# Kernel optimization log

Hardware: AMD Instinct MI355X
Metric: run time of the kernel (lower is better)

## Reference

```python
import jax, jax.numpy as jnp
import numpy as np

N_NODES = 100000


def _gcn_norm(src, dst, n_nodes, n_edges):
    # PyG gcn_norm with add_self_loops=False: deg over target (col) index
    ones = jnp.ones((n_edges,), dtype=jnp.float32)
    deg = jax.ops.segment_sum(ones, dst, num_segments=n_nodes)
    dinv = jnp.where(deg > 0, jax.lax.rsqrt(deg), 0.0)
    return dinv[src] * dinv[dst]  # [E]


def _arma_conv(x, src, dst, ew, init_w, root_w, bias, n_nodes):
    # x: [N, Fin]; init_w/root_w: [K, Fin, Fout]; bias: [K, 1, Fout]
    h = jnp.einsum('nf,kfo->kno', x, init_w)          # [K, N, Fout]
    msg = h[:, src, :] * ew[None, :, None]             # [K, E, Fout]
    agg = jax.vmap(lambda m: jax.ops.segment_sum(m, dst, num_segments=n_nodes))(msg)
    out = agg + jnp.einsum('nf,kfo->kno', x, root_w) + bias
    return jax.nn.relu(out).mean(axis=0)               # mean over stacks K


def setup_inputs() -> dict:
    key = jax.random.key(0)
    ks = jax.random.split(key, 8)
    n, e = N_NODES, 3200000
    nfeat, hid, nclass, K = 512, 16, 40, 2
    x = jax.random.normal(ks[0], (n, nfeat), dtype=jnp.float32)
    edge_index = jax.random.randint(ks[1], (2, e), 0, n, dtype=jnp.int32)
    s1 = (1.0 / np.sqrt(nfeat)).astype(np.float32) if isinstance(np.sqrt(nfeat), np.ndarray) else np.float32(1.0 / np.sqrt(nfeat))
    s2 = np.float32(1.0 / np.sqrt(hid))
    iw1 = jax.random.normal(ks[2], (K, nfeat, hid), dtype=jnp.float32) * s1
    rw1 = jax.random.normal(ks[3], (K, nfeat, hid), dtype=jnp.float32) * s1
    b1 = jax.random.normal(ks[4], (K, 1, hid), dtype=jnp.float32) * 0.01
    iw2 = jax.random.normal(ks[5], (K, hid, nclass), dtype=jnp.float32) * s2
    rw2 = jax.random.normal(ks[6], (K, hid, nclass), dtype=jnp.float32) * s2
    b2 = jax.random.normal(ks[7], (K, 1, nclass), dtype=jnp.float32) * 0.01
    return {'x': x, 'edge_index': edge_index, 'iw1': iw1, 'rw1': rw1, 'b1': b1,
            'iw2': iw2, 'rw2': rw2, 'b2': b2}


def reference(x, edge_index, iw1, rw1, b1, iw2, rw2, b2):
    src, dst = edge_index[0], edge_index[1]
    n = N_NODES
    ew = _gcn_norm(src, dst, n, src.shape[0])
    h = _arma_conv(x, src, dst, ew, iw1, rw1, b1, n)   # [N, 16]
    out = _arma_conv(h, src, dst, ew, iw2, rw2, b2, n) # [N, nclass]
    return out
```

## Files before the change

kernel.cpp:

```cpp
#include <hip/hip_runtime.h>


#define TB 256
#define CHA 4096

typedef __attribute__((ext_vector_type(8))) short bf8;
typedef __attribute__((ext_vector_type(4))) float f4;

__device__ inline unsigned short f2bf_rne(float f) {
  unsigned int u = __float_as_uint(f);
  unsigned int r = u + 0x7fffu + ((u >> 16) & 1u);
  return (unsigned short)(r >> 16);
}
__device__ inline float bf2f(unsigned short h) {
  return __uint_as_float(((unsigned int)h) << 16);
}
__device__ inline float bflo(unsigned int u) { return __uint_as_float(u << 16); }
__device__ inline float bfhi(unsigned int u) { return __uint_as_float(u & 0xffff0000u); }
__device__ inline unsigned int bfpack(float lo, float hi) {
  return (unsigned int)f2bf_rne(lo) | ((unsigned int)f2bf_rne(hi) << 16);
}

__global__ __launch_bounds__(TB) void k_countA(const int* __restrict__ dst,
                                               int* __restrict__ ccnt, int E) {
  __shared__ int cnt[256];
  int tid = threadIdx.x;
  cnt[tid] = 0;
  __syncthreads();
  int e0 = blockIdx.x * CHA;
  int e1 = min(e0 + CHA, E);
  for (int e = e0 + tid; e < e1; e += TB) atomicAdd(&cnt[dst[e] >> 9], 1);
  __syncthreads();
  if (cnt[tid] > 0) atomicAdd(&ccnt[tid], cnt[tid]);
}

__global__ __launch_bounds__(256) void k_scanC(const int* __restrict__ ccnt,
                                               int* __restrict__ cbase,
                                               int* __restrict__ ccur) {
  __shared__ int sh[256];
  int tid = threadIdx.x;
  int v = ccnt[tid];
  sh[tid] = v;
  __syncthreads();
  for (int d = 1; d < 256; d <<= 1) {
    int t = (tid >= d) ? sh[tid - d] : 0;
    __syncthreads();
    sh[tid] += t;
    __syncthreads();
  }
  int excl = sh[tid] - v;
  cbase[tid] = excl;
  ccur[tid] = excl;
  if (tid == 255) cbase[256] = sh[255];
}

__global__ __launch_bounds__(TB) void k_binA(const int* __restrict__ src,
                                             const int* __restrict__ dst,
                                             int* __restrict__ ccur,
                                             int2* __restrict__ epairs, int E) {
  __shared__ int cnt[256];
  __shared__ int gb[256];
  int tid = threadIdx.x;
  cnt[tid] = 0;
  __syncthreads();
  int e0 = blockIdx.x * CHA;
  int e1 = min(e0 + CHA, E);
  for (int e = e0 + tid; e < e1; e += TB) atomicAdd(&cnt[dst[e] >> 9], 1);
  __syncthreads();
  int c = cnt[tid];
  if (c > 0) gb[tid] = atomicAdd(&ccur[tid], c);
  __syncthreads();
  cnt[tid] = 0;
  __syncthreads();
  for (int e = e0 + tid; e < e1; e += TB) {
    int dv = dst[e];
    int b = dv >> 9;
    int r = atomicAdd(&cnt[b], 1);
    epairs[gb[b] + r] = make_int2(src[e], dv);
  }
}

__global__ __launch_bounds__(TB) void k_binB(const int2* __restrict__ epairs,
                                             const int* __restrict__ cbase,
                                             int* __restrict__ degi,
                                             int* __restrict__ offsets,
                                             int* __restrict__ srcs, int N) {
  __shared__ int cnt[512];
  __shared__ int pre[512];
  int b = blockIdx.x;
  int n0 = b << 9;
  int tid = threadIdx.x;
  int beg = cbase[b], end = cbase[b + 1];
  int i0 = tid, i1 = tid + 256;
  cnt[i0] = 0; cnt[i1] = 0;
  __syncthreads();
  for (int e = beg + tid; e < end; e += TB) atomicAdd(&cnt[epairs[e].y - n0], 1);
  __syncthreads();
  pre[i0] = cnt[i0]; pre[i1] = cnt[i1];
  __syncthreads();
  for (int d = 1; d < 512; d <<= 1) {
    int t0 = (i0 >= d) ? pre[i0 - d] : 0;
    int t1 = (i1 >= d) ? pre[i1 - d] : 0;
    __syncthreads();
    pre[i0] += t0; pre[i1] += t1;
    __syncthreads();
  }
  int e0 = pre[i0] - cnt[i0];
  int e1x = pre[i1] - cnt[i1];
  if (n0 + i0 < N) { degi[n0 + i0] = cnt[i0]; offsets[n0 + i0] = beg + e0; }
  if (n0 + i1 < N) { degi[n0 + i1] = cnt[i1]; offsets[n0 + i1] = beg + e1x; }
  __syncthreads();
  cnt[i0] = e0; cnt[i1] = e1x;
  __syncthreads();
  for (int e = beg + tid; e < end; e += TB) {
    int2 p = epairs[e];
    int pos = atomicAdd(&cnt[p.y - n0], 1);
    srcs[beg + pos] = p.x;
  }
}

__global__ __launch_bounds__(TB) void k_dinv(const int* __restrict__ degi,
                                             float* __restrict__ dinv, int N) {
  int i = blockIdx.x * TB + threadIdx.x;
  if (i < N) {
    int d = degi[i];
    dinv[i] = d > 0 ? rsqrtf((float)d) : 0.0f;
  }
}

__global__ __launch_bounds__(TB) void k_wsplit(const float* __restrict__ iw1,
                                               const float* __restrict__ rw1,
                                               short* __restrict__ Whi,
                                               short* __restrict__ Wlo) {
  int idx = blockIdx.x * TB + threadIdx.x;
  if (idx >= 32768) return;
  int j = idx & 7;
  int l = (idx >> 3) & 63;
  int t = (idx >> 9) & 3;
  int c = idx >> 11;
  int k = c * 32 + (l >> 4) * 8 + j;
  int n = t * 16 + (l & 15);
  float w;
  if (n < 16)
    w = iw1[k * 16 + n];
  else if (n < 32)
    w = iw1[8192 + k * 16 + (n - 16)];
  else if (n < 48)
    w = rw1[k * 16 + (n - 32)];
  else
    w = rw1[8192 + k * 16 + (n - 48)];
  unsigned short h = f2bf_rne(w);
  float res = w - bf2f(h);
  Whi[idx] = (short)h;
  Wlo[idx] = (short)f2bf_rne(res);
}

__global__ __launch_bounds__(TB) void k_gemm1_mfma(const float* __restrict__ x,
                                                   const short* __restrict__ Whi,
                                                   const short* __restrict__ Wlo,
                                                   const float* __restrict__ dinv,
                                                   unsigned short* __restrict__ Hs,
                                                   float* __restrict__ R, int N) {
  int lane = threadIdx.x & 63;
  int wave = threadIdx.x >> 6;
  int row0 = blockIdx.x * 64 + wave * 16;
  int m = lane & 15, quad = lane >> 4;
  int r = row0 + m;
  bool rv = (r < N);
  const float* xr = x + (size_t)r * 512;

  f4 acc[4];
#pragma unroll
  for (int t = 0; t < 4; t++) acc[t] = (f4){0.f, 0.f, 0.f, 0.f};

  for (int c = 0; c < 16; ++c) {
    float xv[8];
    if (rv) {
      f4 a0 = *(const f4*)(xr + c * 32 + quad * 8);
      f4 a1 = *(const f4*)(xr + c * 32 + quad * 8 + 4);
      xv[0] = a0.x; xv[1] = a0.y; xv[2] = a0.z; xv[3] = a0.w;
      xv[4] = a1.x; xv[5] = a1.y; xv[6] = a1.z; xv[7] = a1.w;
    } else {
#pragma unroll
      for (int j = 0; j < 8; ++j) xv[j] = 0.f;
    }
    bf8 ahi, alo;
#pragma unroll
    for (int j = 0; j < 8; ++j) {
      unsigned short h = f2bf_rne(xv[j]);
      float res = xv[j] - bf2f(h);
      ahi[j] = (short)h;
      alo[j] = (short)f2bf_rne(res);
    }
    const short* wb = Whi + ((size_t)(c * 4) * 64 + lane) * 8;
    const short* wl = Wlo + ((size_t)(c * 4) * 64 + lane) * 8;
#pragma unroll
    for (int t = 0; t < 4; ++t) {
      bf8 bh = *(const bf8*)(wb + t * 512);
      bf8 bl = *(const bf8*)(wl + t * 512);
      acc[t] = __builtin_amdgcn_mfma_f32_16x16x32_bf16(ahi, bh, acc[t], 0, 0, 0);
      acc[t] = __builtin_amdgcn_mfma_f32_16x16x32_bf16(alo, bh, acc[t], 0, 0, 0);
      acc[t] = __builtin_amdgcn_mfma_f32_16x16x32_bf16(ahi, bl, acc[t], 0, 0, 0);
    }
  }
  float dv[4];
#pragma unroll
  for (int g = 0; g < 4; ++g) {
    int ro = row0 + quad * 4 + g;
    dv[g] = (ro < N) ? dinv[ro] : 0.f;
  }
#pragma unroll
  for (int t = 0; t < 4; ++t) {
#pragma unroll
    for (int g = 0; g < 4; ++g) {
      int ro = row0 + quad * 4 + g;
      if (ro < N) {
        if (t < 2)
          Hs[(size_t)ro * 32 + t * 16 + m] = f2bf_rne(acc[t][g] * dv[g]);
        else
          R[(size_t)ro * 32 + (t - 2) * 16 + m] = acc[t][g];
      }
    }
  }
}

__global__ __launch_bounds__(TB) void k_prop1(const int* __restrict__ offsets,
                                              const int* __restrict__ degi,
                                              const int* __restrict__ srcs,
                                              const unsigned short* __restrict__ Hs,
                                              const float* __restrict__ R,
                                              const float* __restrict__ dinv,
                                              const float* __restrict__ b1,
                                              float* __restrict__ h,
                                              unsigned short* __restrict__ hs, int N) {
  int tid = blockIdx.x * TB + threadIdx.x;
  int q = tid & 3;
  int n = tid >> 2;
  if (n >= N) return;
  int beg = offsets[n], cnt = degi[n];
  float a[8];
#pragma unroll
  for (int j = 0; j < 8; j++) a[j] = 0.f;
  for (int i = 0; i < cnt; i++) {
    int s = srcs[beg + i];
    uint4 v = *(const uint4*)(Hs + (size_t)s * 32 + q * 8);
    a[0] += bflo(v.x); a[1] += bfhi(v.x);
    a[2] += bflo(v.y); a[3] += bfhi(v.y);
    a[4] += bflo(v.z); a[5] += bfhi(v.z);
    a[6] += bflo(v.w); a[7] += bfhi(v.w);
  }
  float dvn = dinv[n];
  f4 r0 = *(const f4*)(R + (size_t)n * 32 + q * 8);
  f4 r1 = *(const f4*)(R + (size_t)n * 32 + q * 8 + 4);
  float rr[8] = {r0.x, r0.y, r0.z, r0.w, r1.x, r1.y, r1.z, r1.w};
  float vv[8];
#pragma unroll
  for (int j = 0; j < 8; j++) {
    int f = q * 8 + j;
    vv[j] = fmaxf(a[j] * dvn + rr[j] + b1[(f >> 4) * 16 + (f & 15)], 0.f);
  }
  float pv[8];
#pragma unroll
  for (int j = 0; j < 8; j++) pv[j] = __shfl_xor(vv[j], 2);
  if (q < 2) {
    float hv[8];
#pragma unroll
    for (int j = 0; j < 8; j++) hv[j] = 0.5f * (vv[j] + pv[j]);
    f4 o0 = {hv[0], hv[1], hv[2], hv[3]};
    f4 o1 = {hv[4], hv[5], hv[6], hv[7]};
    *(f4*)(h + (size_t)n * 16 + q * 8) = o0;
    *(f4*)(h + (size_t)n * 16 + q * 8 + 4) = o1;
    uint4 ob;
    ob.x = bfpack(hv[0] * dvn, hv[1] * dvn);
    ob.y = bfpack(hv[2] * dvn, hv[3] * dvn);
    ob.z = bfpack(hv[4] * dvn, hv[5] * dvn);
    ob.w = bfpack(hv[6] * dvn, hv[7] * dvn);
    *(uint4*)(hs + (size_t)n * 16 + q * 8) = ob;
  }
}

__global__ __launch_bounds__(TB) void k_prop2(const int* __restrict__ offsets,
                                              const int* __restrict__ degi,
                                              const int* __restrict__ srcs,
                                              const unsigned short* __restrict__ hs,
                                              const float* __restrict__ dinv,
                                              float* __restrict__ Ah, int N) {
  int tid = blockIdx.x * TB + threadIdx.x;
  int q = tid & 3;
  int n = tid >> 2;
  if (n >= N) return;
  int beg = offsets[n], cnt = degi[n];
  float a[4] = {0.f, 0.f, 0.f, 0.f};
  for (int i = 0; i < cnt; i++) {
    int s = srcs[beg + i];
    uint2 v = *(const uint2*)(hs + (size_t)s * 16 + q * 4);
    a[0] += bflo(v.x); a[1] += bfhi(v.x);
    a[2] += bflo(v.y); a[3] += bfhi(v.y);
  }
  float dvn = dinv[n];
  f4 o = {a[0] * dvn, a[1] * dvn, a[2] * dvn, a[3] * dvn};
  *(f4*)(Ah + (size_t)n * 16 + q * 4) = o;
}

__global__ __launch_bounds__(TB) void k_final(const float* __restrict__ Ah,
                                              const float* __restrict__ h,
                                              const float* __restrict__ iw2,
                                              const float* __restrict__ rw2,
                                              const float* __restrict__ b2,
                                              float* __restrict__ out, int N) {
  __shared__ float w_iw[2 * 16 * 40];
  __shared__ float w_rw[2 * 16 * 40];
  __shared__ float w_b[2 * 40];
  for (int i = threadIdx.x; i < 1280; i += TB) {
    w_iw[i] = iw2[i];
    w_rw[i] = rw2[i];
  }
  for (int i = threadIdx.x; i < 80; i += TB) w_b[i] = b2[i];
  __syncthreads();

  int idx = blockIdx.x * TB + threadIdx.x;
  if (idx >= N * 40) return;
  int n = idx / 40;
  int o = idx - n * 40;
  float a[16], hr[16];
#pragma unroll
  for (int f = 0; f < 16; f++) {
    a[f] = Ah[(size_t)n * 16 + f];
    hr[f] = h[(size_t)n * 16 + f];
  }
  float res = 0.f;
#pragma unroll
  for (int k = 0; k < 2; k++) {
    float s = w_b[k * 40 + o];
#pragma unroll
    for (int f = 0; f < 16; f++) {
      s += a[f] * w_iw[(k * 16 + f) * 40 + o];
      s += hr[f] * w_rw[(k * 16 + f) * 40 + o];
    }
    res += fmaxf(s, 0.f);
  }
  out[idx] = 0.5f * res;
}

extern "C" void kernel_launch(void* const* d_in, const int* in_sizes, int n_in,
                              void* d_out, int out_size, void* d_ws, size_t ws_size,
                              hipStream_t stream) {
  const float* x = (const float*)d_in[0];
  const int* ei = (const int*)d_in[1];
  const float* iw1 = (const float*)d_in[2];
  const float* rw1 = (const float*)d_in[3];
  const float* b1 = (const float*)d_in[4];
  const float* iw2 = (const float*)d_in[5];
  const float* rw2 = (const float*)d_in[6];
  const float* b2 = (const float*)d_in[7];
  float* out = (float*)d_out;

  const int N = in_sizes[0] / 512;
  const int E = in_sizes[1] / 2;
  const int* src = ei;
  const int* dst = ei + E;
  const int NC = (N + 511) >> 9;

  char* base = (char*)d_ws;
  size_t off = 0;
  auto alloc = [&](size_t bytes) -> void* {
    off = (off + 255) & ~(size_t)255;
    void* p = base + off;
    off += bytes;
    return p;
  };
  int* degi = (int*)alloc((size_t)N * 4);
  float* dinv = (float*)alloc((size_t)N * 4);
  int* offsets = (int*)alloc((size_t)N * 4);
  int* ccnt = (int*)alloc(260 * 4);
  int* cbase = (int*)alloc(260 * 4);
  int* ccur = (int*)alloc(260 * 4);
  int2* epairs = (int2*)alloc((size_t)E * 8);
  int* srcs = (int*)alloc((size_t)E * 4);
  unsigned short* Hs = (unsigned short*)alloc((size_t)N * 32 * 2);
  float* hbuf = (float*)alloc((size_t)N * 16 * 4);
  unsigned short* hs = (unsigned short*)alloc((size_t)N * 16 * 2);
  float* Ah = (float*)alloc((size_t)N * 16 * 4);
  short* Whi = (short*)alloc(32768 * 2);
  short* Wlo = (short*)alloc(32768 * 2);
  float* R = (float*)epairs;
  (void)ws_size;

  hipMemsetAsync(ccnt, 0, 260 * 4, stream);

  int NBLK = (E + CHA - 1) / CHA;
  k_countA<<<NBLK, TB, 0, stream>>>(dst, ccnt, E);
  k_scanC<<<1, 256, 0, stream>>>(ccnt, cbase, ccur);
  k_binA<<<NBLK, TB, 0, stream>>>(src, dst, ccur, epairs, E);
  k_binB<<<NC, TB, 0, stream>>>(epairs, cbase, degi, offsets, srcs, N);
  k_dinv<<<(N + TB - 1) / TB, TB, 0, stream>>>(degi, dinv, N);
  k_wsplit<<<128, TB, 0, stream>>>(iw1, rw1, Whi, Wlo);
  k_gemm1_mfma<<<(N + 63) / 64, TB, 0, stream>>>(x, Whi, Wlo, dinv, Hs, R, N);
  k_prop1<<<((size_t)N * 4 + TB - 1) / TB, TB, 0, stream>>>(offsets, degi, srcs, Hs, R,
                                                            dinv, b1, hbuf, hs, N);
  k_prop2<<<((size_t)N * 4 + TB - 1) / TB, TB, 0, stream>>>(offsets, degi, srcs, hs,
                                                            dinv, Ah, N);
  k_final<<<((size_t)N * 40 + TB - 1) / TB, TB, 0, stream>>>(Ah, hbuf, iw2, rw2, b2, out, N);
}
```

Baseline: 604.2 us.

## Pack edge bins to 32-bit, split CSR scatter, stage neighbor lists in LDS

Each binned edge is now stored as one 32-bit word (local destination in the high bits, source in the low bits) instead of an int2, which halves the binning traffic. The per-bucket scatter moves out of the single-block kernel into a separate 2D-grid kernel that uses global per-node atomic cursors. The degree-inverse computation is folded into the histogram kernel, and R gets its own buffer instead of aliasing the edge buffer. The propagation kernels stage each 64-node block's neighbor indices in LDS and unroll the gather by four for more loads in flight. The risks are that edge order within a node becomes nondeterministic, which can change the float summation order, and that the packing assumes node ids fit in 23 bits.

Measured after the change: 606.7 us. About the same (+0.4%).

```diff
diff --git a/kernel.cpp b/kernel.cpp
--- a/kernel.cpp
+++ b/kernel.cpp
@@ -3,6 +3,7 @@
 
 #define TB 256
 #define CHA 4096
+#define SCAP 4096
 
 typedef __attribute__((ext_vector_type(8))) short bf8;
 typedef __attribute__((ext_vector_type(4))) float f4;
@@ -19,6 +20,16 @@
 __device__ inline float bfhi(unsigned int u) { return __uint_as_float(u & 0xffff0000u); }
 __device__ inline unsigned int bfpack(float lo, float hi) {
   return (unsigned int)f2bf_rne(lo) | ((unsigned int)f2bf_rne(hi) << 16);
+}
+__device__ inline void acc8(float* a, uint4 v) {
+  a[0] += bflo(v.x); a[1] += bfhi(v.x);
+  a[2] += bflo(v.y); a[3] += bfhi(v.y);
+  a[4] += bflo(v.z); a[5] += bfhi(v.z);
+  a[6] += bflo(v.w); a[7] += bfhi(v.w);
+}
+__device__ inline void acc4(float* a, uint2 v) {
+  a[0] += bflo(v.x); a[1] += bfhi(v.x);
+  a[2] += bflo(v.y); a[3] += bfhi(v.y);
 }
 
 __global__ __launch_bounds__(TB) void k_countA(const int* __restrict__ dst,
@@ -57,7 +68,7 @@
 __global__ __launch_bounds__(TB) void k_binA(const int* __restrict__ src,
                                              const int* __restrict__ dst,
                                              int* __restrict__ ccur,
-                                             int2* __restrict__ epairs, int E) {
+                                             unsigned int* __restrict__ epack, int E) {
   __shared__ int cnt[256];
   __shared__ int gb[256];
   int tid = threadIdx.x;
@@ -76,15 +87,16 @@
     int dv = dst[e];
     int b = dv >> 9;
     int r = atomicAdd(&cnt[b], 1);
-    epairs[gb[b] + r] = make_int2(src[e], dv);
-  }
-}
-
-__global__ __launch_bounds__(TB) void k_binB(const int2* __restrict__ epairs,
+    epack[gb[b] + r] = ((unsigned int)(dv & 511) << 23) | (unsigned int)src[e];
+  }
+}
+
+__global__ __launch_bounds__(TB) void k_hist(const unsigned int* __restrict__ epack,
                                              const int* __restrict__ cbase,
                                              int* __restrict__ degi,
                                              int* __restrict__ offsets,
-                                             int* __restrict__ srcs, int N) {
+                                             int* __restrict__ cursor,
+                                             float* __restrict__ dinv, int N) {
   __shared__ int cnt[512];
   __shared__ int pre[512];
   int b = blockIdx.x;
@@ -94,7 +106,7 @@
   int i0 = tid, i1 = tid + 256;
   cnt[i0] = 0; cnt[i1] = 0;
   __syncthreads();
-  for (int e = beg + tid; e < end; e += TB) atomicAdd(&cnt[epairs[e].y - n0], 1);
+  for (int e = beg + tid; e < end; e += TB) atomicAdd(&cnt[epack[e] >> 23], 1);
   __syncthreads();
   pre[i0] = cnt[i0]; pre[i1] = cnt[i1];
   __syncthreads();
@@ -107,24 +119,34 @@
   }
   int e0 = pre[i0] - cnt[i0];
   int e1x = pre[i1] - cnt[i1];
-  if (n0 + i0 < N) { degi[n0 + i0] = cnt[i0]; offsets[n0 + i0] = beg + e0; }
-  if (n0 + i1 < N) { degi[n0 + i1] = cnt[i1]; offsets[n0 + i1] = beg + e1x; }
-  __syncthreads();
-  cnt[i0] = e0; cnt[i1] = e1x;
-  __syncthreads();
-  for (int e = beg + tid; e < end; e += TB) {
-    int2 p = epairs[e];
-    int pos = atomicAdd(&cnt[p.y - n0], 1);
-    srcs[beg + pos] = p.x;
-  }
-}
-
-__global__ __launch_bounds__(TB) void k_dinv(const int* __restrict__ degi,
-                                             float* __restrict__ dinv, int N) {
-  int i = blockIdx.x * TB + threadIdx.x;
-  if (i < N) {
-    int d = degi[i];
-    dinv[i] = d > 0 ? rsqrtf((float)d) : 0.0f;
+  if (n0 + i0 < N) {
+    int c = cnt[i0];
+    degi[n0 + i0] = c; offsets[n0 + i0] = beg + e0; cursor[n0 + i0] = beg + e0;
+    dinv[n0 + i0] = c > 0 ? rsqrtf((float)c) : 0.f;
+  }
+  if (n0 + i1 < N) {
+    int c = cnt[i1];
+    degi[n0 + i1] = c; offsets[n0 + i1] = beg + e1x; cursor[n0 + i1] = beg + e1x;
+    dinv[n0 + i1] = c > 0 ? rsqrtf((float)c) : 0.f;
+  }
+}
+
+__global__ __launch_bounds__(TB) void k_scat(const unsigned int* __restrict__ epack,
+                                             const int* __restrict__ cbase,
+                                             int* __restrict__ cursor,
+                                             int* __restrict__ srcs) {
+  int b = blockIdx.x;
+  int beg = cbase[b], end = cbase[b + 1];
+  int len = end - beg;
+  int ny = (int)gridDim.y;
+  int chunk = (len + ny - 1) / ny;
+  int lo = beg + blockIdx.y * chunk;
+  int hi = min(lo + chunk, end);
+  for (int e = lo + (int)threadIdx.x; e < hi; e += TB) {
+    unsigned int v = epack[e];
+    int node = (b << 9) + (int)(v >> 23);
+    int pos = atomicAdd(&cursor[node], 1);
+    srcs[pos] = (int)(v & 0x7FFFFFu);
   }
 }
 
@@ -232,22 +254,53 @@
                                               const float* __restrict__ dinv,
                                               const float* __restrict__ b1,
                                               float* __restrict__ h,
-                                              unsigned short* __restrict__ hs, int N) {
-  int tid = blockIdx.x * TB + threadIdx.x;
+                                              unsigned short* __restrict__ hs,
+                                              int N, int E) {
+  __shared__ int sh[SCAP];
+  int n0 = blockIdx.x * 64;
+  int tid = threadIdx.x;
   int q = tid & 3;
-  int n = tid >> 2;
+  int n = n0 + (tid >> 2);
+  int beg0 = offsets[n0];
+  int end0 = (n0 + 64 < N) ? offsets[n0 + 64] : E;
+  int seg = end0 - beg0;
+  bool lds_ok = (seg <= SCAP);
+  if (lds_ok) {
+    for (int i = tid; i < seg; i += TB) sh[i] = srcs[beg0 + i];
+  }
+  __syncthreads();
   if (n >= N) return;
   int beg = offsets[n], cnt = degi[n];
-  float a[8];
-#pragma unroll
-  for (int j = 0; j < 8; j++) a[j] = 0.f;
-  for (int i = 0; i < cnt; i++) {
-    int s = srcs[beg + i];
-    uint4 v = *(const uint4*)(Hs + (size_t)s * 32 + q * 8);
-    a[0] += bflo(v.x); a[1] += bfhi(v.x);
-    a[2] += bflo(v.y); a[3] += bfhi(v.y);
-    a[4] += bflo(v.z); a[5] += bfhi(v.z);
-    a[6] += bflo(v.w); a[7] += bfhi(v.w);
+  const unsigned short* Hsq = Hs + q * 8;
+  float a[8] = {0.f, 0.f, 0.f, 0.f, 0.f, 0.f, 0.f, 0.f};
+  int i = 0;
+  if (lds_ok) {
+    int ib = beg - beg0;
+    for (; i + 4 <= cnt; i += 4) {
+      int s0 = sh[ib + i], s1 = sh[ib + i + 1], s2 = sh[ib + i + 2], s3 = sh[ib + i + 3];
+      uint4 v0 = *(const uint4*)(Hsq + (size_t)s0 * 32);
+      uint4 v1 = *(const uint4*)(Hsq + (size_t)s1 * 32);
+      uint4 v2 = *(const uint4*)(Hsq + (size_t)s2 * 32);
+      uint4 v3 = *(const uint4*)(Hsq + (size_t)s3 * 32);
+      acc8(a, v0); acc8(a, v1); acc8(a, v2); acc8(a, v3);
+    }
+    for (; i < cnt; i++) {
+      uint4 v = *(const uint4*)(Hsq + (size_t)sh[ib + i] * 32);
+      acc8(a, v);
+    }
+  } else {
+    for (; i + 4 <= cnt; i += 4) {
+      int s0 = srcs[beg + i], s1 = srcs[beg + i + 1], s2 = srcs[beg + i + 2], s3 = srcs[beg + i + 3];
+      uint4 v0 = *(const uint4*)(Hsq + (size_t)s0 * 32);
+      uint4 v1 = *(const uint4*)(Hsq + (size_t)s1 * 32);
+      uint4 v2 = *(const uint4*)(Hsq + (size_t)s2 * 32);
+      uint4 v3 = *(const uint4*)(Hsq + (size_t)s3 * 32);
+      acc8(a, v0); acc8(a, v1); acc8(a, v2); acc8(a, v3);
+    }
+    for (; i < cnt; i++) {
+      uint4 v = *(const uint4*)(Hsq + (size_t)srcs[beg + i] * 32);
+      acc8(a, v);
+    }
   }
   float dvn = dinv[n];
   f4 r0 = *(const f4*)(R + (size_t)n * 32 + q * 8);
@@ -255,10 +308,8 @@
   float rr[8] = {r0.x, r0.y, r0.z, r0.w, r1.x, r1.y, r1.z, r1.w};
   float vv[8];
 #pragma unroll
-  for (int j = 0; j < 8; j++) {
-    int f = q * 8 + j;
-    vv[j] = fmaxf(a[j] * dvn + rr[j] + b1[(f >> 4) * 16 + (f & 15)], 0.f);
-  }
+  for (int j = 0; j < 8; j++)
+    vv[j] = fmaxf(a[j] * dvn + rr[j] + b1[q * 8 + j], 0.f);
   float pv[8];
 #pragma unroll
   for (int j = 0; j < 8; j++) pv[j] = __shfl_xor(vv[j], 2);
@@ -284,18 +335,52 @@
                                               const int* __restrict__ srcs,
                                               const unsigned short* __restrict__ hs,
                                               const float* __restrict__ dinv,
-                                              float* __restrict__ Ah, int N) {
-  int tid = blockIdx.x * TB + threadIdx.x;
+                                              float* __restrict__ Ah, int N, int E) {
+  __shared__ int sh[SCAP];
+  int n0 = blockIdx.x * 64;
+  int tid = threadIdx.x;
   int q = tid & 3;
-  int n = tid >> 2;
+  int n = n0 + (tid >> 2);
+  int beg0 = offsets[n0];
+  int end0 = (n0 + 64 < N) ? offsets[n0 + 64] : E;
+  int seg = end0 - beg0;
+  bool lds_ok = (seg <= SCAP);
+  if (lds_ok) {
+    for (int i = tid; i < seg; i += TB) sh[i] = srcs[beg0 + i];
+  }
+  __syncthreads();
   if (n >= N) return;
   int beg = offsets[n], cnt = degi[n];
+  const unsigned short* hq = hs + q * 4;
   float a[4] = {0.f, 0.f, 0.f, 0.f};
-  for (int i = 0; i < cnt; i++) {
-    int s = srcs[beg + i];
-    uint2 v = *(const uint2*)(hs + (size_t)s * 16 + q * 4);
-    a[0] += bflo(v.x); a[1] += bfhi(v.x);
-    a[2] += bflo(v.y); a[3] += bfhi(v.y);
+  int i = 0;
+  if (lds_ok) {
+    int ib = beg - beg0;
+    for (; i + 4 <= cnt; i += 4) {
+      int s0 = sh[ib + i], s1 = sh[ib + i + 1], s2 = sh[ib + i + 2], s3 = sh[ib + i + 3];
+      uint2 v0 = *(const uint2*)(hq + (size_t)s0 * 16);
+      uint2 v1 = *(const uint2*)(hq + (size_t)s1 * 16);
+      uint2 v2 = *(const uint2*)(hq + (size_t)s2 * 16);
+      uint2 v3 = *(const uint2*)(hq + (size_t)s3 * 16);
+      acc4(a, v0); acc4(a, v1); acc4(a, v2); acc4(a, v3);
+    }
+    for (; i < cnt; i++) {
+      uint2 v = *(const uint2*)(hq + (size_t)sh[ib + i] * 16);
+      acc4(a, v);
+    }
+  } else {
+    for (; i + 4 <= cnt; i += 4) {
+      int s0 = srcs[beg + i], s1 = srcs[beg + i + 1], s2 = srcs[beg + i + 2], s3 = srcs[beg + i + 3];
+      uint2 v0 = *(const uint2*)(hq + (size_t)s0 * 16);
+      uint2 v1 = *(const uint2*)(hq + (size_t)s1 * 16);
+      uint2 v2 = *(const uint2*)(hq + (size_t)s2 * 16);
+      uint2 v3 = *(const uint2*)(hq + (size_t)s3 * 16);
+      acc4(a, v0); acc4(a, v1); acc4(a, v2); acc4(a, v3);
+    }
+    for (; i < cnt; i++) {
+      uint2 v = *(const uint2*)(hq + (size_t)srcs[beg + i] * 16);
+      acc4(a, v);
+    }
   }
   float dvn = dinv[n];
   f4 o = {a[0] * dvn, a[1] * dvn, a[2] * dvn, a[3] * dvn};
@@ -372,33 +457,33 @@
   int* degi = (int*)alloc((size_t)N * 4);
   float* dinv = (float*)alloc((size_t)N * 4);
   int* offsets = (int*)alloc((size_t)N * 4);
+  int* cursor = (int*)alloc((size_t)N * 4);
   int* ccnt = (int*)alloc(260 * 4);
   int* cbase = (int*)alloc(260 * 4);
   int* ccur = (int*)alloc(260 * 4);
-  int2* epairs = (int2*)alloc((size_t)E * 8);
+  unsigned int* epack = (unsigned int*)alloc((size_t)E * 4);
   int* srcs = (int*)alloc((size_t)E * 4);
   unsigned short* Hs = (unsigned short*)alloc((size_t)N * 32 * 2);
+  float* R = (float*)alloc((size_t)N * 32 * 4);
   float* hbuf = (float*)alloc((size_t)N * 16 * 4);
   unsigned short* hs = (unsigned short*)alloc((size_t)N * 16 * 2);
   float* Ah = (float*)alloc((size_t)N * 16 * 4);
   short* Whi = (short*)alloc(32768 * 2);
   short* Wlo = (short*)alloc(32768 * 2);
-  float* R = (float*)epairs;
   (void)ws_size;
 
   hipMemsetAsync(ccnt, 0, 260 * 4, stream);
 
   int NBLK = (E + CHA - 1) / CHA;
+  int NPB = (N + 63) / 64;
   k_countA<<<NBLK, TB, 0, stream>>>(dst, ccnt, E);
   k_scanC<<<1, 256, 0, stream>>>(ccnt, cbase, ccur);
-  k_binA<<<NBLK, TB, 0, stream>>>(src, dst, ccur, epairs, E);
-  k_binB<<<NC, TB, 0, stream>>>(epairs, cbase, degi, offsets, srcs, N);
-  k_dinv<<<(N + TB - 1) / TB, TB, 0, stream>>>(degi, dinv, N);
+  k_binA<<<NBLK, TB, 0, stream>>>(src, dst, ccur, epack, E);
+  k_hist<<<NC, TB, 0, stream>>>(epack, cbase, degi, offsets, cursor, dinv, N);
+  k_scat<<<dim3(NC, 8), TB, 0, stream>>>(epack, cbase, cursor, srcs);
   k_wsplit<<<128, TB, 0, stream>>>(iw1, rw1, Whi, Wlo);
   k_gemm1_mfma<<<(N + 63) / 64, TB, 0, stream>>>(x, Whi, Wlo, dinv, Hs, R, N);
-  k_prop1<<<((size_t)N * 4 + TB - 1) / TB, TB, 0, stream>>>(offsets, degi, srcs, Hs, R,
-                                                            dinv, b1, hbuf, hs, N);
-  k_prop2<<<((size_t)N * 4 + TB - 1) / TB, TB, 0, stream>>>(offsets, degi, srcs, hs,
-                                                            dinv, Ah, N);
+  k_prop1<<<NPB, TB, 0, stream>>>(offsets, degi, srcs, Hs, R, dinv, b1, hbuf, hs, N, E);
+  k_prop2<<<NPB, TB, 0, stream>>>(offsets, degi, srcs, hs, dinv, Ah, N, E);
   k_final<<<((size_t)N * 40 + TB - 1) / TB, TB, 0, stream>>>(Ah, hbuf, iw2, rw2, b2, out, N);
 }
```
